# Performance work log

Hardware: AMD Instinct MI355X
Metric: run time of the kernel (lower is better)

The kernel has to match this reference:

```python
import jax, jax.numpy as jnp
import numpy as np


def setup_inputs() -> dict:
    key = jax.random.key(0)
    k1, k2, k3, k4 = jax.random.split(key, 4)
    n_smps, n_fcns, d_in, d_out = 16384, 2048, 32, 32
    GAIN = 1e-5  # xavier gain used by init_wts / init_offsets
    x = jax.random.normal(k1, (n_smps, d_in), dtype=jnp.float32)
    ctrs = jax.random.normal(k2, (n_fcns, d_in), dtype=jnp.float32)
    wts = jax.random.normal(k3, (n_fcns, d_in, d_out), dtype=jnp.float32) * GAIN
    offsets = jax.random.normal(k4, (n_fcns, d_out), dtype=jnp.float32) * GAIN
    return {"x": x, "ctrs": ctrs, "wts": wts, "offsets": offsets, "k": 4}


def reference(x, ctrs, wts, offsets, k):
    # --- knn_do equivalent (done under no_grad in torch) ---
    # squared Euclidean distance: (n_smps, n_fcns)
    x_sg = jax.lax.stop_gradient(x)
    c_sg = jax.lax.stop_gradient(ctrs)
    d2 = (jnp.sum(x_sg * x_sg, axis=1, keepdims=True)
          - 2.0 * (x_sg @ c_sg.T)
          + jnp.sum(c_sg * c_sg, axis=1)[None, :])
    _, idx = jax.lax.top_k(-d2, k)  # (n_smps, k), nearest centers

    # --- gather per-neighbor local linear models ---
    sel_wts = wts[idx]        # (n_smps, k, d_in, d_out)
    sel_ctrs = ctrs[idx]      # (n_smps, k, d_in)
    sel_offs = offsets[idx]   # (n_smps, k, d_out)

    applied_wts = jnp.sum(sel_wts, axis=1)  # (n_smps, d_in, d_out)
    # offsets minus sum over neighbors/d_in of wts * ctrs
    applied_offsets = (jnp.sum(sel_offs, axis=1)
                       - jnp.einsum('nkde,nkd->ne', sel_wts, sel_ctrs))
    # y = x @ applied_wts + applied_offsets, per sample
    y = jnp.einsum('nde,nd->ne', applied_wts, x) + applied_offsets
    return y
```

## Files before the change

### kernel.cpp

```cpp
#include <hip/hip_runtime.h>
#include <math.h>

typedef short bf16x8 __attribute__((ext_vector_type(8)));
typedef float f32x4  __attribute__((ext_vector_type(4)));

#define N_SMPS 16384
#define N_FCNS 2048
#define D_IN 32
#define D_OUT 32
#define KNN 4
#define SPLITS 4
#define CPS 512
#define TILES 32
#define POOL 48
#define PPOOL 49
#define SMP 16

__device__ __forceinline__ unsigned umin_u(unsigned a, unsigned b) { return a < b ? a : b; }
__device__ __forceinline__ unsigned umax_u(unsigned a, unsigned b) { return a > b ? a : b; }

__device__ __forceinline__ unsigned short bf16_rne(float f) {
  unsigned b = __float_as_uint(f);
  unsigned r = b + 0x7FFFu + ((b >> 16) & 1u);
  return (unsigned short)(r >> 16);
}

#define OFF_XH   0u
#define OFF_CH   1048576u
#define OFF_HB   (OFF_CH + 131072u)
#define OFF_WB   (OFF_HB + 8192u)

#define NX4 (N_SMPS * D_IN / 4)
#define NC4 (N_FCNS * D_IN / 4)
#define NW4 (N_FCNS * D_IN * D_OUT / 4)
#define NTOT (NX4 + NC4 + NW4)

__global__ __launch_bounds__(256) void k_prep(
    const float* __restrict__ x, const float* __restrict__ ctrs,
    const float* __restrict__ wts,
    unsigned short* __restrict__ xh, unsigned short* __restrict__ ch,
    unsigned short* __restrict__ wb, float* __restrict__ hb)
{
  const int gt = blockIdx.x * 256 + threadIdx.x;
  const float* src; unsigned short* dst; int i4;
  if (gt < NX4)            { src = x;    dst = xh; i4 = gt; }
  else if (gt < NX4 + NC4) { src = ctrs; dst = ch; i4 = gt - NX4; }
  else                     { src = wts;  dst = wb; i4 = gt - (NX4 + NC4); }
  float4 v = ((const float4*)src)[i4];
  ushort4 o;
  o.x = bf16_rne(v.x); o.y = bf16_rne(v.y);
  o.z = bf16_rne(v.z); o.w = bf16_rne(v.w);
  ((ushort4*)dst)[i4] = o;

  if (gt < N_FCNS) {
    const float4* cp4 = (const float4*)(ctrs + (size_t)gt * D_IN);
    float a = 0.f;
    #pragma unroll
    for (int q = 0; q < 8; ++q) {
      float4 c = cp4[q];
      a += c.x * c.x + c.y * c.y + c.z * c.z + c.w * c.w;
    }
    hb[gt] = -0.5f * a;
  }
}

__global__ __launch_bounds__(256) void k_mega(
    const unsigned short* __restrict__ xh, const unsigned short* __restrict__ ch,
    const float* __restrict__ hb,
    const float* __restrict__ x, const float* __restrict__ ctrs,
    const unsigned short* __restrict__ wb, const float* __restrict__ offs,
    float* __restrict__ y)
{
  __shared__ __align__(16) char u_mem[16640];
  __shared__ float    s_hb[SPLITS * CPS + 2048];
  __shared__ unsigned s_pool[SMP][POOL];
  __shared__ int      s_sel[SMP][KNN];

  unsigned* s_cand = (unsigned*)u_mem;
  double*   s_pd2  = (double*)u_mem;
  int*      s_pix  = (int*)(u_mem + 6272);
  float*    s_diff = (float*)u_mem;
  float4*   s_part = (float4*)(u_mem + 8448);

  const int tid = threadIdx.x;
  const int lane = tid & 63;
  const int w = __builtin_amdgcn_readfirstlane(tid >> 6);
  const int col = lane & 15;
  const int quad = lane >> 4;
  const int sbase = blockIdx.x * SMP;
  const int nbase0 = w * CPS;

  #pragma unroll
  for (int r = 0; r < CPS / 64; ++r)
    s_hb[nbase0 + r * 64 + lane] = hb[nbase0 + r * 64 + lane];

  const bf16x8 ah =
      *(const bf16x8*)(xh + (size_t)(sbase + col) * D_IN + quad * 8);

  unsigned ls[4][4];
  #pragma unroll
  for (int r = 0; r < 4; ++r)
    #pragma unroll
    for (int e = 0; e < 4; ++e) ls[r][e] = 0u;

  const unsigned short* chb =
      ch + (size_t)nbase0 * D_IN + (size_t)col * D_IN + quad * 8;
  #define BLOAD(t) (*(const bf16x8*)(chb + (size_t)(t) * 16 * D_IN))
  #define HLOAD(t) (s_hb[nbase0 + (t) * 16 + col])

  __syncthreads();

  bf16x8 bh[4];
  float  hv[4];
  #pragma unroll
  for (int p = 0; p < 4; ++p) { bh[p] = BLOAD(p); hv[p] = HLOAD(p); }

  for (int t = 0; t < TILES; t += 4) {
    #pragma unroll
    for (int p = 0; p < 4; ++p) {
      {
        f32x4 acc = {0.f, 0.f, 0.f, 0.f};
        acc = __builtin_amdgcn_mfma_f32_16x16x32_bf16(ah, bh[p], acc, 0, 0, 0);
        const unsigned tc = (unsigned)((t + p) * 16 + col);
        const float hvv = hv[p];
        #pragma unroll
        for (int r = 0; r < 4; ++r) {
          const float uu = acc[r] + hvv;
          unsigned b = __float_as_uint(uu);
          unsigned m = b ^ ((unsigned)((int)b >> 31) | 0x80000000u);
          unsigned key = (m & 0xFFFFFE00u) | tc;
          unsigned t0 = umin_u(ls[r][0], key); ls[r][0] = umax_u(ls[r][0], key);
          unsigned t1 = umin_u(ls[r][1], t0);  ls[r][1] = umax_u(ls[r][1], t0);
          unsigned t2 = umin_u(ls[r][2], t1);  ls[r][2] = umax_u(ls[r][2], t1);
          ls[r][3] = umax_u(ls[r][3], t2);
        }
      }
      const int tn = (t + 4 + p) & (TILES - 1);
      bh[p] = BLOAD(tn);
      hv[p] = HLOAD(tn);
    }
  }
  #undef BLOAD
  #undef HLOAD

  #pragma unroll
  for (int r = 0; r < 4; ++r) {
    const int row = quad * 4 + r;
    *(uint4*)&s_cand[(((w * 16) + row) * 16 + (col ^ row)) * 4] =
        make_uint4(ls[r][0], ls[r][1], ls[r][2], ls[r][3]);
  }
  __syncthreads();

  if (tid < 128) {
    const int sl = tid >> 3;
    const int g  = tid & 7;
    const int wv = g >> 1;
    const int chh = (g & 1) * 8;
    unsigned q0 = 0, q1 = 0, q2 = 0, q3 = 0, q4 = 0, q5 = 0;
    #pragma unroll
    for (int c2 = 0; c2 < 8; ++c2) {
      uint4 kv = *(const uint4*)
          &s_cand[(((wv * 16) + sl) * 16 + ((chh + c2) ^ sl)) * 4];
      unsigned ks[4] = {kv.x, kv.y, kv.z, kv.w};
      #pragma unroll
      for (int e = 0; e < 4; ++e) {
        unsigned key = ks[e];
        unsigned t0 = umin_u(q0, key); q0 = umax_u(q0, key);
        unsigned t1 = umin_u(q1, t0);  q1 = umax_u(q1, t0);
        unsigned t2 = umin_u(q2, t1);  q2 = umax_u(q2, t1);
        unsigned t3 = umin_u(q3, t2);  q3 = umax_u(q3, t2);
        unsigned t4 = umin_u(q4, t3);  q4 = umax_u(q4, t3);
        q5 = umax_u(q5, t4);
      }
    }
    unsigned* op = &s_pool[sl][g * 6];
    op[0] = q0; op[1] = q1; op[2] = q2;
    op[3] = q3; op[4] = q4; op[5] = q5;
  }
  __syncthreads();

  for (int c = tid; c < SMP * POOL; c += 256) {
    const int sl = c / POOL;
    const int p = c - sl * POOL;
    const unsigned key = s_pool[sl][p];
    const int wv = p / 12;
    const int j = wv * CPS + (int)(key & 0x1FFu);
    const float4* xp4 = (const float4*)(x + (size_t)(sbase + sl) * D_IN);
    const float4* cp4 = (const float4*)(ctrs + (size_t)j * D_IN);
    double d2a = 0.0, d2b = 0.0;
    #pragma unroll
    for (int q = 0; q < 8; ++q) {
      float4 cv = cp4[q];
      float4 xv = xp4[q];
      double df0 = (double)xv.x - (double)cv.x;
      double df1 = (double)xv.y - (double)cv.y;
      double df2 = (double)xv.z - (double)cv.z;
      double df3 = (double)xv.w - (double)cv.w;
      d2a = fma(df0, df0, d2a);
      d2b = fma(df1, df1, d2b);
      d2a = fma(df2, df2, d2a);
      d2b = fma(df3, df3, d2b);
    }
    s_pd2[sl * PPOOL + p] = d2a + d2b;
    s_pix[sl * PPOOL + p] = j;
  }
  __syncthreads();

  if (tid < SMP) {
    double bd[4]; int b4[4];
    #pragma unroll
    for (int e = 0; e < 4; ++e) { bd[e] = 1e300; b4[e] = 0x7fffffff; }
    for (int m = 0; m < POOL; ++m) {
      const double d2 = s_pd2[tid * PPOOL + m];
      const int j = s_pix[tid * PPOOL + m];
      bool ins = (d2 < bd[3]) || (d2 == bd[3] && j < b4[3]);
      if (ins) {
        bd[3] = d2; b4[3] = j;
        #pragma unroll
        for (int q = 3; q > 0; --q) {
          bool sw = (bd[q] < bd[q - 1]) ||
                    (bd[q] == bd[q - 1] && b4[q] < b4[q - 1]);
          if (sw) {
            double td = bd[q]; bd[q] = bd[q - 1]; bd[q - 1] = td;
            int    tj = b4[q]; b4[q] = b4[q - 1]; b4[q - 1] = tj;
          }
        }
      }
    }
    #pragma unroll
    for (int q = 0; q < 4; ++q) s_sel[tid][q] = b4[q];
  }
  __syncthreads();

  #pragma unroll
  for (int r = 0; r < SMP * KNN * D_IN / 256; ++r) {
    int v = r * 256 + tid;
    int d = v & 31; int p = v >> 5;
    int sl = p >> 2; int j = p & 3;
    int f = s_sel[sl][j];
    s_diff[(sl * KNN + j) * (D_IN + 1) + d] =
        x[(size_t)(sbase + sl) * D_IN + d] - ctrs[(size_t)f * D_IN + d];
  }
  __syncthreads();

  #pragma unroll
  for (int r = 0; r < 2; ++r) {
    const int slot = r * 256 + tid;
    const int sl = slot >> 5;
    const int j  = (slot >> 3) & 3;
    const int eq = slot & 7;
    const int f = s_sel[sl][j];
    const uint2* wp = (const uint2*)(wb + (size_t)f * (D_IN * D_OUT));
    float4 acc = ((const float4*)(offs + (size_t)f * D_OUT))[eq];
    #pragma unroll
    for (int d = 0; d < D_IN; ++d) {
      uint2 wv = wp[d * 8 + eq];
      float w0 = __uint_as_float(wv.x << 16);
      float w1 = __uint_as_float(wv.x & 0xFFFF0000u);
      float w2 = __uint_as_float(wv.y << 16);
      float w3 = __uint_as_float(wv.y & 0xFFFF0000u);
      float xc = s_diff[(sl * KNN + j) * (D_IN + 1) + d];
      acc.x = fmaf(xc, w0, acc.x);
      acc.y = fmaf(xc, w1, acc.y);
      acc.z = fmaf(xc, w2, acc.z);
      acc.w = fmaf(xc, w3, acc.w);
    }
    s_part[(sl * KNN + j) * 8 + eq] = acc;
  }
  __syncthreads();

  #pragma unroll
  for (int r = 0; r < 2; ++r) {
    const int slot = r * 256 + tid;
    const int sl = slot >> 5;
    const int j  = (slot >> 3) & 3;
    const int eq = slot & 7;
    if (j == 0) {
      float4 a = s_part[(sl * KNN + 0) * 8 + eq];
      float4 b = s_part[(sl * KNN + 1) * 8 + eq];
      float4 c = s_part[(sl * KNN + 2) * 8 + eq];
      float4 e = s_part[(sl * KNN + 3) * 8 + eq];
      float4 o;
      o.x = (a.x + b.x) + (c.x + e.x);
      o.y = (a.y + b.y) + (c.y + e.y);
      o.z = (a.z + b.z) + (c.z + e.z);
      o.w = (a.w + b.w) + (c.w + e.w);
      ((float4*)(y + (size_t)(sbase + sl) * D_OUT))[eq] = o;
    }
  }
}

extern "C" void kernel_launch(void* const* d_in, const int* in_sizes, int n_in,
                              void* d_out, int out_size, void* d_ws, size_t ws_size,
                              hipStream_t stream) {
  const float* x    = (const float*)d_in[0];
  const float* ctrs = (const float*)d_in[1];
  const float* wts  = (const float*)d_in[2];
  const float* offs = (const float*)d_in[3];
  float* y = (float*)d_out;

  char* ws = (char*)d_ws;
  unsigned short* xh = (unsigned short*)(ws + OFF_XH);
  unsigned short* ch = (unsigned short*)(ws + OFF_CH);
  float*          hb = (float*)(ws + OFF_HB);
  unsigned short* wb = (unsigned short*)(ws + OFF_WB);

  k_prep<<<NTOT / 256, 256, 0, stream>>>(x, ctrs, wts, xh, ch, wb, hb);
  k_mega<<<N_SMPS / SMP, 256, 0, stream>>>(xh, ch, hb, x, ctrs, wb, offs, y);
}
```

Baseline: 112.0 us.

## Split fused kNN kernel into top-k and finish kernels with global candidate pool

Splits the single fused kernel into a candidate-selection kernel and a refinement/apply kernel. Each top-k block now scans half the centers with 16-tile loops, which doubles the block count, and writes 6 candidate indices per wave per sample to a global pool. The finish kernel processes 8 samples per block for more parallelism in the exact-distance and weight-application phases. This trades an extra launch and a global round trip of the candidate pool for shorter per-block critical paths and better occupancy.

```diff
diff --git a/kernel.cpp b/kernel.cpp
--- a/kernel.cpp
+++ b/kernel.cpp
@@ -9,12 +9,13 @@
 #define D_IN 32
 #define D_OUT 32
 #define KNN 4
-#define SPLITS 4
-#define CPS 512
-#define TILES 32
+#define SMP 16
+#define FSMP 8
+#define HALF 1024
+#define WCT 256
+#define TILES 16
 #define POOL 48
 #define PPOOL 49
-#define SMP 16
 
 __device__ __forceinline__ unsigned umin_u(unsigned a, unsigned b) { return a < b ? a : b; }
 __device__ __forceinline__ unsigned umax_u(unsigned a, unsigned b) { return a > b ? a : b; }
@@ -29,6 +30,7 @@
 #define OFF_CH   1048576u
 #define OFF_HB   (OFF_CH + 131072u)
 #define OFF_WB   (OFF_HB + 8192u)
+#define OFF_PL   (OFF_WB + 8388608u)
 
 #define NX4 (N_SMPS * D_IN / 4)
 #define NC4 (N_FCNS * D_IN / 4)
@@ -64,35 +66,26 @@
   }
 }
 
-__global__ __launch_bounds__(256) void k_mega(
+__global__ __launch_bounds__(256) void k_topk(
     const unsigned short* __restrict__ xh, const unsigned short* __restrict__ ch,
-    const float* __restrict__ hb,
-    const float* __restrict__ x, const float* __restrict__ ctrs,
-    const unsigned short* __restrict__ wb, const float* __restrict__ offs,
-    float* __restrict__ y)
+    const float* __restrict__ hb, unsigned short* __restrict__ pool)
 {
-  __shared__ __align__(16) char u_mem[16640];
-  __shared__ float    s_hb[SPLITS * CPS + 2048];
-  __shared__ unsigned s_pool[SMP][POOL];
-  __shared__ int      s_sel[SMP][KNN];
-
-  unsigned* s_cand = (unsigned*)u_mem;
-  double*   s_pd2  = (double*)u_mem;
-  int*      s_pix  = (int*)(u_mem + 6272);
-  float*    s_diff = (float*)u_mem;
-  float4*   s_part = (float4*)(u_mem + 8448);
+  __shared__ __align__(16) unsigned s_cand[2 * 16 * 16 * 4];
+  __shared__ float s_hb[4 * WCT];
 
   const int tid = threadIdx.x;
   const int lane = tid & 63;
   const int w = __builtin_amdgcn_readfirstlane(tid >> 6);
   const int col = lane & 15;
   const int quad = lane >> 4;
-  const int sbase = blockIdx.x * SMP;
-  const int nbase0 = w * CPS;
-
-  #pragma unroll
-  for (int r = 0; r < CPS / 64; ++r)
-    s_hb[nbase0 + r * 64 + lane] = hb[nbase0 + r * 64 + lane];
+  const int sg = blockIdx.x >> 1;
+  const int h  = blockIdx.x & 1;
+  const int sbase = sg * SMP;
+  const int nbase = h * HALF + w * WCT;
+
+  #pragma unroll
+  for (int r = 0; r < WCT / 64; ++r)
+    s_hb[w * WCT + r * 64 + lane] = hb[nbase + r * 64 + lane];
 
   const bf16x8 ah =
       *(const bf16x8*)(xh + (size_t)(sbase + col) * D_IN + quad * 8);
@@ -104,9 +97,9 @@
     for (int e = 0; e < 4; ++e) ls[r][e] = 0u;
 
   const unsigned short* chb =
-      ch + (size_t)nbase0 * D_IN + (size_t)col * D_IN + quad * 8;
+      ch + (size_t)nbase * D_IN + (size_t)col * D_IN + quad * 8;
   #define BLOAD(t) (*(const bf16x8*)(chb + (size_t)(t) * 16 * D_IN))
-  #define HLOAD(t) (s_hb[nbase0 + (t) * 16 + col])
+  #define HLOAD(t) (s_hb[w * WCT + (t) * 16 + col])
 
   __syncthreads();
 
@@ -128,7 +121,7 @@
           const float uu = acc[r] + hvv;
           unsigned b = __float_as_uint(uu);
           unsigned m = b ^ ((unsigned)((int)b >> 31) | 0x80000000u);
-          unsigned key = (m & 0xFFFFFE00u) | tc;
+          unsigned key = (m & 0xFFFFFF00u) | tc;
           unsigned t0 = umin_u(ls[r][0], key); ls[r][0] = umax_u(ls[r][0], key);
           unsigned t1 = umin_u(ls[r][1], t0);  ls[r][1] = umax_u(ls[r][1], t0);
           unsigned t2 = umin_u(ls[r][2], t1);  ls[r][2] = umax_u(ls[r][2], t1);
@@ -144,47 +137,71 @@
   #undef HLOAD
 
   #pragma unroll
-  for (int r = 0; r < 4; ++r) {
-    const int row = quad * 4 + r;
-    *(uint4*)&s_cand[(((w * 16) + row) * 16 + (col ^ row)) * 4] =
-        make_uint4(ls[r][0], ls[r][1], ls[r][2], ls[r][3]);
-  }
-  __syncthreads();
-
-  if (tid < 128) {
-    const int sl = tid >> 3;
-    const int g  = tid & 7;
-    const int wv = g >> 1;
-    const int chh = (g & 1) * 8;
-    unsigned q0 = 0, q1 = 0, q2 = 0, q3 = 0, q4 = 0, q5 = 0;
-    #pragma unroll
-    for (int c2 = 0; c2 < 8; ++c2) {
-      uint4 kv = *(const uint4*)
-          &s_cand[(((wv * 16) + sl) * 16 + ((chh + c2) ^ sl)) * 4];
-      unsigned ks[4] = {kv.x, kv.y, kv.z, kv.w};
+  for (int sh = 0; sh < 2; ++sh) {
+    if ((w >> 1) == sh) {
+      const int slw = w & 1;
       #pragma unroll
-      for (int e = 0; e < 4; ++e) {
-        unsigned key = ks[e];
-        unsigned t0 = umin_u(q0, key); q0 = umax_u(q0, key);
-        unsigned t1 = umin_u(q1, t0);  q1 = umax_u(q1, t0);
-        unsigned t2 = umin_u(q2, t1);  q2 = umax_u(q2, t1);
-        unsigned t3 = umin_u(q3, t2);  q3 = umax_u(q3, t2);
-        unsigned t4 = umin_u(q4, t3);  q4 = umax_u(q4, t3);
-        q5 = umax_u(q5, t4);
+      for (int r = 0; r < 4; ++r) {
+        const int row = quad * 4 + r;
+        *(uint4*)&s_cand[(((slw * 16) + row) * 16 + (col ^ row)) * 4] =
+            make_uint4(ls[r][0], ls[r][1], ls[r][2], ls[r][3]);
       }
     }
-    unsigned* op = &s_pool[sl][g * 6];
-    op[0] = q0; op[1] = q1; op[2] = q2;
-    op[3] = q3; op[4] = q4; op[5] = q5;
-  }
-  __syncthreads();
-
-  for (int c = tid; c < SMP * POOL; c += 256) {
+    __syncthreads();
+    if (tid < 32) {
+      const int sl = tid >> 1;
+      const int slot = tid & 1;
+      unsigned q0 = 0, q1 = 0, q2 = 0, q3 = 0, q4 = 0, q5 = 0;
+      #pragma unroll
+      for (int c2 = 0; c2 < 16; ++c2) {
+        uint4 kv = *(const uint4*)
+            &s_cand[(((slot * 16) + sl) * 16 + (c2 ^ sl)) * 4];
+        unsigned ks[4] = {kv.x, kv.y, kv.z, kv.w};
+        #pragma unroll
+        for (int e = 0; e < 4; ++e) {
+          unsigned key = ks[e];
+          unsigned t0 = umin_u(q0, key); q0 = umax_u(q0, key);
+          unsigned t1 = umin_u(q1, t0);  q1 = umax_u(q1, t0);
+          unsigned t2 = umin_u(q2, t1);  q2 = umax_u(q2, t1);
+          unsigned t3 = umin_u(q3, t2);  q3 = umax_u(q3, t2);
+          unsigned t4 = umin_u(q4, t3);  q4 = umax_u(q4, t3);
+          q5 = umax_u(q5, t4);
+        }
+      }
+      const int wv = sh * 2 + slot;
+      const unsigned jb = (unsigned)(h * HALF + wv * WCT);
+      unsigned short* gp =
+          pool + (size_t)(sbase + sl) * POOL + (size_t)(h * 4 + wv) * 6;
+      gp[0] = (unsigned short)(jb + (q0 & 0xFFu));
+      gp[1] = (unsigned short)(jb + (q1 & 0xFFu));
+      gp[2] = (unsigned short)(jb + (q2 & 0xFFu));
+      gp[3] = (unsigned short)(jb + (q3 & 0xFFu));
+      gp[4] = (unsigned short)(jb + (q4 & 0xFFu));
+      gp[5] = (unsigned short)(jb + (q5 & 0xFFu));
+    }
+    __syncthreads();
+  }
+}
+
+__global__ __launch_bounds__(256, 8) void k_finish(
+    const unsigned short* __restrict__ pool,
+    const float* __restrict__ x, const float* __restrict__ ctrs,
+    const unsigned short* __restrict__ wb, const float* __restrict__ offs,
+    float* __restrict__ y)
+{
+  __shared__ double s_pd2[FSMP * PPOOL];
+  __shared__ int    s_pix[FSMP * PPOOL];
+  __shared__ int    s_sel[FSMP][KNN];
+  __shared__ float  s_diff[FSMP * KNN * (D_IN + 1)];
+  __shared__ __align__(16) float4 s_part[FSMP * KNN * 8];
+
+  const int tid = threadIdx.x;
+  const int sbase = blockIdx.x * FSMP;
+
+  for (int c = tid; c < FSMP * POOL; c += 256) {
     const int sl = c / POOL;
     const int p = c - sl * POOL;
-    const unsigned key = s_pool[sl][p];
-    const int wv = p / 12;
-    const int j = wv * CPS + (int)(key & 0x1FFu);
+    const int j = (int)pool[(size_t)(sbase + sl) * POOL + p];
     const float4* xp4 = (const float4*)(x + (size_t)(sbase + sl) * D_IN);
     const float4* cp4 = (const float4*)(ctrs + (size_t)j * D_IN);
     double d2a = 0.0, d2b = 0.0;
@@ -206,7 +223,7 @@
   }
   __syncthreads();
 
-  if (tid < SMP) {
+  if (tid < FSMP) {
     double bd[4]; int b4[4];
     #pragma unroll
     for (int e = 0; e < 4; ++e) { bd[e] = 1e300; b4[e] = 0x7fffffff; }
@@ -233,7 +250,7 @@
   __syncthreads();
 
   #pragma unroll
-  for (int r = 0; r < SMP * KNN * D_IN / 256; ++r) {
+  for (int r = 0; r < FSMP * KNN * D_IN / 256; ++r) {
     int v = r * 256 + tid;
     int d = v & 31; int p = v >> 5;
     int sl = p >> 2; int j = p & 3;
@@ -243,12 +260,10 @@
   }
   __syncthreads();
 
-  #pragma unroll
-  for (int r = 0; r < 2; ++r) {
-    const int slot = r * 256 + tid;
-    const int sl = slot >> 5;
-    const int j  = (slot >> 3) & 3;
-    const int eq = slot & 7;
+  {
+    const int sl = tid >> 5;
+    const int j  = (tid >> 3) & 3;
+    const int eq = tid & 7;
     const int f = s_sel[sl][j];
     const uint2* wp = (const uint2*)(wb + (size_t)f * (D_IN * D_OUT));
     float4 acc = ((const float4*)(offs + (size_t)f * D_OUT))[eq];
@@ -269,12 +284,10 @@
   }
   __syncthreads();
 
-  #pragma unroll
-  for (int r = 0; r < 2; ++r) {
-    const int slot = r * 256 + tid;
-    const int sl = slot >> 5;
-    const int j  = (slot >> 3) & 3;
-    const int eq = slot & 7;
+  {
+    const int sl = tid >> 5;
+    const int j  = (tid >> 3) & 3;
+    const int eq = tid & 7;
     if (j == 0) {
       float4 a = s_part[(sl * KNN + 0) * 8 + eq];
       float4 b = s_part[(sl * KNN + 1) * 8 + eq];
@@ -304,7 +317,9 @@
   unsigned short* ch = (unsigned short*)(ws + OFF_CH);
   float*          hb = (float*)(ws + OFF_HB);
   unsigned short* wb = (unsigned short*)(ws + OFF_WB);
+  unsigned short* pl = (unsigned short*)(ws + OFF_PL);
 
   k_prep<<<NTOT / 256, 256, 0, stream>>>(x, ctrs, wts, xh, ch, wb, hb);
-  k_mega<<<N_SMPS / SMP, 256, 0, stream>>>(xh, ch, hb, x, ctrs, wb, offs, y);
-}
+  k_topk<<<(N_SMPS / SMP) * 2, 256, 0, stream>>>(xh, ch, hb, pl);
+  k_finish<<<N_SMPS / FSMP, 256, 0, stream>>>(pl, x, ctrs, wb, offs, y);
+}
```

New measurement: 121.5 us. 1.08x slower.

## Fuse prep and main kernels into one cooperative launch with grid sync

Applied to the files above, without the earlier changes.

Merges the bf16 conversion/prep kernel and the main kNN+apply kernel into a single cooperative kernel of 1024 blocks. Prep work is done in a grid-stride loop, followed by a threadfence and a grid-wide sync. This removes one kernel launch and the gap between the two kernels. The cost is a grid barrier and reliance on all 1024 blocks being co-resident, with a fallback to the two-kernel path if the cooperative launch fails.

```diff
diff --git a/kernel.cpp b/kernel.cpp
--- a/kernel.cpp
+++ b/kernel.cpp
@@ -1,5 +1,8 @@
 #include <hip/hip_runtime.h>
+#include <hip/hip_cooperative_groups.h>
 #include <math.h>
+
+namespace cg = cooperative_groups;
 
 typedef short bf16x8 __attribute__((ext_vector_type(8)));
 typedef float f32x4  __attribute__((ext_vector_type(4)));
@@ -15,6 +18,7 @@
 #define POOL 48
 #define PPOOL 49
 #define SMP 16
+#define GRID 1024
 
 __device__ __forceinline__ unsigned umin_u(unsigned a, unsigned b) { return a < b ? a : b; }
 __device__ __forceinline__ unsigned umax_u(unsigned a, unsigned b) { return a > b ? a : b; }
@@ -35,47 +39,42 @@
 #define NW4 (N_FCNS * D_IN * D_OUT / 4)
 #define NTOT (NX4 + NC4 + NW4)
 
-__global__ __launch_bounds__(256) void k_prep(
-    const float* __restrict__ x, const float* __restrict__ ctrs,
+__device__ __forceinline__ void prep_slot(
+    int g, const float* __restrict__ x, const float* __restrict__ ctrs,
     const float* __restrict__ wts,
     unsigned short* __restrict__ xh, unsigned short* __restrict__ ch,
     unsigned short* __restrict__ wb, float* __restrict__ hb)
 {
-  const int gt = blockIdx.x * 256 + threadIdx.x;
   const float* src; unsigned short* dst; int i4;
-  if (gt < NX4)            { src = x;    dst = xh; i4 = gt; }
-  else if (gt < NX4 + NC4) { src = ctrs; dst = ch; i4 = gt - NX4; }
-  else                     { src = wts;  dst = wb; i4 = gt - (NX4 + NC4); }
+  if (g < NX4)            { src = x;    dst = xh; i4 = g; }
+  else if (g < NX4 + NC4) { src = ctrs; dst = ch; i4 = g - NX4; }
+  else                    { src = wts;  dst = wb; i4 = g - (NX4 + NC4); }
   float4 v = ((const float4*)src)[i4];
   ushort4 o;
   o.x = bf16_rne(v.x); o.y = bf16_rne(v.y);
   o.z = bf16_rne(v.z); o.w = bf16_rne(v.w);
   ((ushort4*)dst)[i4] = o;
 
-  if (gt < N_FCNS) {
-    const float4* cp4 = (const float4*)(ctrs + (size_t)gt * D_IN);
+  if (g < N_FCNS) {
+    const float4* cp4 = (const float4*)(ctrs + (size_t)g * D_IN);
     float a = 0.f;
     #pragma unroll
     for (int q = 0; q < 8; ++q) {
       float4 c = cp4[q];
       a += c.x * c.x + c.y * c.y + c.z * c.z + c.w * c.w;
     }
-    hb[gt] = -0.5f * a;
-  }
-}
-
-__global__ __launch_bounds__(256) void k_mega(
+    hb[g] = -0.5f * a;
+  }
+}
+
+__device__ __forceinline__ void mega_body(
     const unsigned short* __restrict__ xh, const unsigned short* __restrict__ ch,
     const float* __restrict__ hb,
     const float* __restrict__ x, const float* __restrict__ ctrs,
     const unsigned short* __restrict__ wb, const float* __restrict__ offs,
-    float* __restrict__ y)
-{
-  __shared__ __align__(16) char u_mem[16640];
-  __shared__ float    s_hb[SPLITS * CPS + 2048];
-  __shared__ unsigned s_pool[SMP][POOL];
-  __shared__ int      s_sel[SMP][KNN];
-
+    float* __restrict__ y,
+    char* u_mem, float* s_hb, unsigned (*s_pool)[POOL], int (*s_sel)[KNN])
+{
   unsigned* s_cand = (unsigned*)u_mem;
   double*   s_pd2  = (double*)u_mem;
   int*      s_pix  = (int*)(u_mem + 6272);
@@ -290,6 +289,52 @@
   }
 }
 
+__global__ __launch_bounds__(256) void k_fused(
+    unsigned short* __restrict__ xh, unsigned short* __restrict__ ch,
+    float* __restrict__ hb,
+    const float* __restrict__ x, const float* __restrict__ ctrs,
+    const float* __restrict__ wts,
+    unsigned short* __restrict__ wb, const float* __restrict__ offs,
+    float* __restrict__ y)
+{
+  __shared__ __align__(16) char u_mem[16640];
+  __shared__ float    s_hb[SPLITS * CPS + 2048];
+  __shared__ unsigned s_pool[SMP][POOL];
+  __shared__ int      s_sel[SMP][KNN];
+
+  for (int g = blockIdx.x * 256 + threadIdx.x; g < NTOT; g += GRID * 256)
+    prep_slot(g, x, ctrs, wts, xh, ch, wb, hb);
+
+  __threadfence();
+  cg::this_grid().sync();
+
+  mega_body(xh, ch, hb, x, ctrs, wb, offs, y, u_mem, s_hb, s_pool, s_sel);
+}
+
+__global__ __launch_bounds__(256) void k_prep(
+    const float* __restrict__ x, const float* __restrict__ ctrs,
+    const float* __restrict__ wts,
+    unsigned short* __restrict__ xh, unsigned short* __restrict__ ch,
+    unsigned short* __restrict__ wb, float* __restrict__ hb)
+{
+  const int gt = blockIdx.x * 256 + threadIdx.x;
+  prep_slot(gt, x, ctrs, wts, xh, ch, wb, hb);
+}
+
+__global__ __launch_bounds__(256) void k_mega(
+    const unsigned short* __restrict__ xh, const unsigned short* __restrict__ ch,
+    const float* __restrict__ hb,
+    const float* __restrict__ x, const float* __restrict__ ctrs,
+    const unsigned short* __restrict__ wb, const float* __restrict__ offs,
+    float* __restrict__ y)
+{
+  __shared__ __align__(16) char u_mem[16640];
+  __shared__ float    s_hb[SPLITS * CPS + 2048];
+  __shared__ unsigned s_pool[SMP][POOL];
+  __shared__ int      s_sel[SMP][KNN];
+  mega_body(xh, ch, hb, x, ctrs, wb, offs, y, u_mem, s_hb, s_pool, s_sel);
+}
+
 extern "C" void kernel_launch(void* const* d_in, const int* in_sizes, int n_in,
                               void* d_out, int out_size, void* d_ws, size_t ws_size,
                               hipStream_t stream) {
@@ -305,6 +350,13 @@
   float*          hb = (float*)(ws + OFF_HB);
   unsigned short* wb = (unsigned short*)(ws + OFF_WB);
 
-  k_prep<<<NTOT / 256, 256, 0, stream>>>(x, ctrs, wts, xh, ch, wb, hb);
-  k_mega<<<N_SMPS / SMP, 256, 0, stream>>>(xh, ch, hb, x, ctrs, wb, offs, y);
-}
+  void* args[] = { (void*)&xh, (void*)&ch, (void*)&hb, (void*)&x, (void*)&ctrs,
+                   (void*)&wts, (void*)&wb, (void*)&offs, (void*)&y };
+  hipError_t rc = hipLaunchCooperativeKernel(
+      (const void*)k_fused, dim3(GRID), dim3(256), args, 0, stream);
+
+  if (rc != hipSuccess) {
+    k_prep<<<NTOT / 256, 256, 0, stream>>>(x, ctrs, wts, xh, ch, wb, hb);
+    k_mega<<<N_SMPS / SMP, 256, 0, stream>>>(xh, ch, hb, x, ctrs, wb, offs, y);
+  }
+}
```

After: 315.7 us. 2.82x slower.

## Make candidate pooling wave-local to drop block-wide barriers

Applied to the files above, without the earlier changes.

Each wave now merges its own candidate lists and computes exact fp64 distances only for its own split of centers. This removes three __syncthreads barriers between the MFMA scan, the merge and the rescoring stages. The pd2/pix scratch gets its own shared buffer so it no longer aliases s_cand, and s_hb shrinks to hold only the bias values. The initial barrier after loading s_hb is dropped, which is only safe because each wave reads back just the region it wrote. The merge stage now uses half-waves instead of two full waves, which trades some per-wave parallelism for the removed syncs.

```diff
diff --git a/kernel.cpp b/kernel.cpp
--- a/kernel.cpp
+++ b/kernel.cpp
@@ -72,13 +72,14 @@
     float* __restrict__ y)
 {
   __shared__ __align__(16) char u_mem[16640];
-  __shared__ float    s_hb[SPLITS * CPS + 2048];
+  __shared__ __align__(16) char pdpx[9408];
+  __shared__ float    s_hb[SPLITS * CPS];
   __shared__ unsigned s_pool[SMP][POOL];
   __shared__ int      s_sel[SMP][KNN];
 
   unsigned* s_cand = (unsigned*)u_mem;
-  double*   s_pd2  = (double*)u_mem;
-  int*      s_pix  = (int*)(u_mem + 6272);
+  double*   s_pd2  = (double*)pdpx;
+  int*      s_pix  = (int*)(pdpx + 6272);
   float*    s_diff = (float*)u_mem;
   float4*   s_part = (float4*)(u_mem + 8448);
 
@@ -107,8 +108,6 @@
       ch + (size_t)nbase0 * D_IN + (size_t)col * D_IN + quad * 8;
   #define BLOAD(t) (*(const bf16x8*)(chb + (size_t)(t) * 16 * D_IN))
   #define HLOAD(t) (s_hb[nbase0 + (t) * 16 + col])
-
-  __syncthreads();
 
   bf16x8 bh[4];
   float  hv[4];
@@ -149,18 +148,17 @@
     *(uint4*)&s_cand[(((w * 16) + row) * 16 + (col ^ row)) * 4] =
         make_uint4(ls[r][0], ls[r][1], ls[r][2], ls[r][3]);
   }
-  __syncthreads();
-
-  if (tid < 128) {
-    const int sl = tid >> 3;
-    const int g  = tid & 7;
-    const int wv = g >> 1;
-    const int chh = (g & 1) * 8;
+
+  if (lane < 32) {
+    const int sl = lane >> 1;
+    const int half = lane & 1;
+    const int g = w * 2 + half;
+    const int chh = half * 8;
     unsigned q0 = 0, q1 = 0, q2 = 0, q3 = 0, q4 = 0, q5 = 0;
     #pragma unroll
     for (int c2 = 0; c2 < 8; ++c2) {
       uint4 kv = *(const uint4*)
-          &s_cand[(((wv * 16) + sl) * 16 + ((chh + c2) ^ sl)) * 4];
+          &s_cand[(((w * 16) + sl) * 16 + ((chh + c2) ^ sl)) * 4];
       unsigned ks[4] = {kv.x, kv.y, kv.z, kv.w};
       #pragma unroll
       for (int e = 0; e < 4; ++e) {
@@ -177,14 +175,13 @@
     op[0] = q0; op[1] = q1; op[2] = q2;
     op[3] = q3; op[4] = q4; op[5] = q5;
   }
-  __syncthreads();
-
-  for (int c = tid; c < SMP * POOL; c += 256) {
-    const int sl = c / POOL;
-    const int p = c - sl * POOL;
+
+  for (int c = lane; c < SMP * 12; c += 64) {
+    const int sl = c / 12;
+    const int pl = c - sl * 12;
+    const int p = w * 12 + pl;
     const unsigned key = s_pool[sl][p];
-    const int wv = p / 12;
-    const int j = wv * CPS + (int)(key & 0x1FFu);
+    const int j = nbase0 + (int)(key & 0x1FFu);
     const float4* xp4 = (const float4*)(x + (size_t)(sbase + sl) * D_IN);
     const float4* cp4 = (const float4*)(ctrs + (size_t)j * D_IN);
     double d2a = 0.0, d2b = 0.0;
```

After: 111.5 us. About the same (-0.5%).
